# Kernel optimization log

Measured on AMD Instinct MI355X. Metric: run time of the kernel, lower is better.

The kernel has to match this reference:

```python
import jax, jax.numpy as jnp
import numpy as np

B, T, D = 2, 2048, 1024
H, KVH, HD = 16, 4, 64  # query heads, kv heads, head_dim
GROUPS = H // KVH


def apply_rope(x, cos, sin):
    # x: (B, nh, T, hd); cos/sin: (max_T, hd//2)
    t = x.shape[2]
    c = cos[:t][None, None]  # (1,1,T,hd//2)
    s = sin[:t][None, None]
    half = x.shape[-1] // 2
    x1, x2 = x[..., :half], x[..., half:]
    rotated = jnp.concatenate((-x2, x1), axis=-1)
    cf = jnp.concatenate((c, c), axis=-1)  # repeat(1,1,1,2)
    sf = jnp.concatenate((s, s), axis=-1)
    return x * cf + rotated * sf


def setup_inputs():
    key = jax.random.key(0)
    ks = jax.random.split(key, 5)
    x = jax.random.normal(ks[0], (B, T, D), dtype=jnp.float32)
    # RoPE tables: theta^(-i/half) frequencies
    half = HD // 2
    inv_freq = 1.0 / (10000.0 ** (jnp.arange(half, dtype=jnp.float32) / half))
    ang = jnp.arange(T, dtype=jnp.float32)[:, None] * inv_freq[None, :]  # (T, half)
    rope_cos = jnp.cos(ang)
    rope_sin = jnp.sin(ang)
    # Causal additive mask
    causal = jnp.tril(jnp.ones((T, T), dtype=bool))
    attention_mask = jnp.where(causal, 0.0, -1e9).astype(jnp.float32)[None, None]
    scale = 0.02
    Wq = jax.random.normal(ks[1], (D, D), dtype=jnp.float32) * scale
    Wk = jax.random.normal(ks[2], (D, KVH * HD), dtype=jnp.float32) * scale
    Wv = jax.random.normal(ks[3], (D, KVH * HD), dtype=jnp.float32) * scale
    Wo = jax.random.normal(ks[4], (D, D), dtype=jnp.float32) * scale
    return {"x": x, "rope_cos": rope_cos, "rope_sin": rope_sin,
            "attention_mask": attention_mask,
            "Wq": Wq, "Wk": Wk, "Wv": Wv, "Wo": Wo}


def reference(x, rope_cos, rope_sin, attention_mask, Wq, Wk, Wv, Wo):
    b, t, _ = x.shape
    q = (x @ Wq).reshape(b, t, H, HD).transpose(0, 2, 1, 3)      # (B,H,T,hd)
    k = (x @ Wk).reshape(b, t, KVH, HD).transpose(0, 2, 1, 3)    # (B,KVH,T,hd)
    v = (x @ Wv).reshape(b, t, KVH, HD).transpose(0, 2, 1, 3)
    q = apply_rope(q, rope_cos, rope_sin)
    k = apply_rope(k, rope_cos, rope_sin)
    if GROUPS > 1:
        k = jnp.repeat(k, GROUPS, axis=1)  # repeat_interleave over heads
        v = jnp.repeat(v, GROUPS, axis=1)
    scale = 1.0 / np.sqrt(HD)
    attn = jnp.einsum('bhqd,bhkd->bhqk', q, k) * scale
    attn = attn + attention_mask
    attn = jax.nn.softmax(attn.astype(jnp.float32), axis=-1).astype(q.dtype)
    out = jnp.einsum('bhqk,bhkd->bhqd', attn, v)
    out = out.transpose(0, 2, 1, 3).reshape(b, t, D)
    return out @ Wo
```

## Files before the change

kernel.cpp:

```cpp
#include <hip/hip_runtime.h>

typedef __attribute__((ext_vector_type(8))) short short8;
typedef __attribute__((ext_vector_type(4))) short short4v;
typedef __attribute__((ext_vector_type(4))) float f32x4;
typedef __attribute__((ext_vector_type(16))) float f32x16;
typedef __attribute__((ext_vector_type(2))) unsigned uint2v;
typedef __attribute__((ext_vector_type(4))) unsigned uint4v;

#define T_ 2048
#define H_ 16
#define KVH_ 4
#define QSCALE 0.18033688011112042f
#define DEFER 8.0f

__device__ inline unsigned short f2bf(float f) {
    unsigned u = __builtin_bit_cast(unsigned, f);
    u += 0x7fff + ((u >> 16) & 1);
    return (unsigned short)(u >> 16);
}
__device__ inline float bf2f(unsigned short v) {
    unsigned u = ((unsigned)v) << 16;
    return __builtin_bit_cast(float, u);
}
__device__ inline unsigned pk2(float lo, float hi) {
    unsigned r;
    asm("v_cvt_pk_bf16_f32 %0, %1, %2" : "=v"(r) : "v"(lo), "v"(hi));
    return r;
}

__device__ inline void gl_lds16(const unsigned short* g, unsigned short* lds) {
    __builtin_amdgcn_global_load_lds(
        (const __attribute__((address_space(1))) unsigned int*)g,
        (__attribute__((address_space(3))) unsigned int*)lds, 16, 0, 0);
}

__device__ void tr_tile(const float* __restrict__ W, unsigned short* __restrict__ out,
                        int K, int N, int rowoff, int bx, int by, int tid,
                        unsigned short (*ts)[66]) {
    #pragma unroll
    for (int s = 0; s < 16; ++s) {
        int idx = tid + s * 256;
        int kl = idx >> 6, nl = idx & 63;
        ts[kl][nl] = f2bf(W[(size_t)(by * 64 + kl) * N + bx * 64 + nl]);
    }
    __syncthreads();
    #pragma unroll
    for (int s = 0; s < 16; ++s) {
        int idx = tid + s * 256;
        int nl = idx >> 6, kl = idx & 63;
        out[(size_t)(rowoff + bx * 64 + nl) * K + by * 64 + kl] = ts[kl][nl];
    }
}

__global__ __launch_bounds__(256) void prep_fused(
        const float* __restrict__ x,
        const float* __restrict__ Wq, const float* __restrict__ Wk,
        const float* __restrict__ Wv, const float* __restrict__ Wo,
        unsigned short* __restrict__ xb, unsigned short* __restrict__ Wt,
        unsigned short* __restrict__ Wot) {
    __shared__ unsigned short ts[64][66];
    const int bid = blockIdx.x, tid = threadIdx.x;
    if (bid < 2048) {
        int i = bid * 256 + tid;
        float4 v0 = ((const float4*)x)[i * 2];
        float4 v1 = ((const float4*)x)[i * 2 + 1];
        short8 o;
        o[0] = f2bf(v0.x); o[1] = f2bf(v0.y); o[2] = f2bf(v0.z); o[3] = f2bf(v0.w);
        o[4] = f2bf(v1.x); o[5] = f2bf(v1.y); o[6] = f2bf(v1.z); o[7] = f2bf(v1.w);
        ((short8*)xb)[i] = o;
    } else if (bid < 2304) {
        int t = bid - 2048;
        tr_tile(Wq, Wt, 1024, 1024, 0, t & 15, t >> 4, tid, ts);
    } else if (bid < 2368) {
        int t = bid - 2304;
        tr_tile(Wk, Wt, 1024, 256, 1024, t & 3, t >> 2, tid, ts);
    } else if (bid < 2432) {
        int t = bid - 2368;
        tr_tile(Wv, Wt, 1024, 256, 1280, t & 3, t >> 2, tid, ts);
    } else {
        int t = bid - 2432;
        tr_tile(Wo, Wot, 1024, 1024, 0, t & 15, t >> 4, tid, ts);
    }
}

__global__ __launch_bounds__(256) void gemm_qkv(
        const unsigned short* __restrict__ A,
        const unsigned short* __restrict__ Bt,
        unsigned short* __restrict__ Cq, unsigned short* __restrict__ Ck,
        unsigned short* __restrict__ Cvt,
        const float* __restrict__ rc, const float* __restrict__ rs) {
    const int K = 1024;
    __shared__ __align__(16) unsigned short As[128 * 32];
    __shared__ __align__(16) unsigned short Bs[128 * 32];
    const int tid = threadIdx.x;
    const int w = tid >> 6, l = tid & 63, lk = l & 15, lg = l >> 4;
    const int wr = w >> 1, wc = w & 1;
    const int bx = blockIdx.x, by = blockIdx.y;

    const unsigned short* Arow = A + (size_t)by * 128 * K;
    const unsigned short* Brow = Bt + (size_t)bx * 128 * K;

    f32x4 acc[4][4];
    #pragma unroll
    for (int m = 0; m < 4; ++m)
        #pragma unroll
        for (int n = 0; n < 4; ++n) acc[m][n] = (f32x4){0, 0, 0, 0};

    for (int k0 = 0; k0 < K; k0 += 32) {
        #pragma unroll
        for (int p = 0; p < 2; ++p) {
            int cb = w * 64 + p * 256;
            int c = cb + l;
            int row = c >> 2, ko = (c & 3) * 8;
            gl_lds16(Arow + (size_t)row * K + k0 + ko, As + cb * 8);
            gl_lds16(Brow + (size_t)row * K + k0 + ko, Bs + cb * 8);
        }
        __syncthreads();
        short8 aF[4], bF[4];
        #pragma unroll
        for (int m = 0; m < 4; ++m)
            aF[m] = *(const short8*)&As[(wr * 64 + m * 16 + lk) * 32 + lg * 8];
        #pragma unroll
        for (int n = 0; n < 4; ++n)
            bF[n] = *(const short8*)&Bs[(wc * 64 + n * 16 + lk) * 32 + lg * 8];
        #pragma unroll
        for (int m = 0; m < 4; ++m)
            #pragma unroll
            for (int n = 0; n < 4; ++n)
                acc[m][n] = __builtin_amdgcn_mfma_f32_16x16x32_bf16(
                    aF[m], bF[n], acc[m][n], 0, 0, 0);
        __syncthreads();
    }

    const int rowbase = by * 128 + wr * 64;
    const int colgrp = bx * 2 + wc;
    if (colgrp < 16) {
        const int h = colgrp;
        #pragma unroll
        for (int m = 0; m < 4; ++m)
            #pragma unroll
            for (int r = 0; r < 4; ++r) {
                int trow = rowbase + m * 16 + lg * 4 + r;
                int b = trow >> 11, t = trow & (T_ - 1);
                size_t ob = (((size_t)(b * 16 + h)) * T_ + t) * 64;
                #pragma unroll
                for (int n = 0; n < 2; ++n) {
                    int d = n * 16 + lk;
                    float cc = rc[t * 32 + d], ss = rs[t * 32 + d];
                    float x1 = acc[m][n][r], x2 = acc[m][n + 2][r];
                    Cq[ob + d]      = f2bf((x1 * cc - x2 * ss) * QSCALE);
                    Cq[ob + d + 32] = f2bf((x2 * cc + x1 * ss) * QSCALE);
                }
            }
    } else if (colgrp < 20) {
        const int kvh = colgrp - 16;
        #pragma unroll
        for (int m = 0; m < 4; ++m)
            #pragma unroll
            for (int r = 0; r < 4; ++r) {
                int trow = rowbase + m * 16 + lg * 4 + r;
                int b = trow >> 11, t = trow & (T_ - 1);
                size_t ob = (((size_t)(b * 4 + kvh)) * T_ + t) * 64;
                #pragma unroll
                for (int n = 0; n < 2; ++n) {
                    int d = n * 16 + lk;
                    float cc = rc[t * 32 + d], ss = rs[t * 32 + d];
                    float x1 = acc[m][n][r], x2 = acc[m][n + 2][r];
                    Ck[ob + d]      = f2bf(x1 * cc - x2 * ss);
                    Ck[ob + d + 32] = f2bf(x2 * cc + x1 * ss);
                }
            }
    } else {
        const int kvh = colgrp - 20;
        #pragma unroll
        for (int m = 0; m < 4; ++m) {
            int trow0 = rowbase + m * 16 + lg * 4;
            int b = trow0 >> 11, t0 = trow0 & (T_ - 1);
            #pragma unroll
            for (int n = 0; n < 4; ++n) {
                int d = n * 16 + lk;
                short4v pk;
                #pragma unroll
                for (int r = 0; r < 4; ++r) pk[r] = f2bf(acc[m][n][r]);
                *(short4v*)(Cvt + (((size_t)(b * 4 + kvh)) * 64 + d) * T_ + t0) = pk;
            }
        }
    }
}

__global__ __launch_bounds__(256) void gemm_o(
        const unsigned short* __restrict__ A,
        const unsigned short* __restrict__ Bt,
        float* __restrict__ C, int M, int N, int K) {
    __shared__ __align__(16) unsigned short As[128 * 32];
    __shared__ __align__(16) unsigned short Bs[64 * 32];
    const int tid = threadIdx.x;
    const int w = tid >> 6, l = tid & 63, lk = l & 15, lg = l >> 4;
    const int bx = blockIdx.x, by = blockIdx.y;

    const unsigned short* Arow = A + (size_t)by * 128 * K;
    const unsigned short* Brow = Bt + (size_t)bx * 64 * K;

    f32x4 acc[2][4];
    #pragma unroll
    for (int m = 0; m < 2; ++m)
        #pragma unroll
        for (int n = 0; n < 4; ++n) acc[m][n] = (f32x4){0, 0, 0, 0};

    for (int k0 = 0; k0 < K; k0 += 32) {
        #pragma unroll
        for (int p = 0; p < 2; ++p) {
            int cb = p * 256 + w * 64;
            int c = cb + l;
            int row = c >> 2, ko = (c & 3) * 8;
            gl_lds16(Arow + (size_t)row * K + k0 + ko, As + cb * 8);
        }
        {
            int c = w * 64 + l;
            int row = c >> 2, ko = (c & 3) * 8;
            gl_lds16(Brow + (size_t)row * K + k0 + ko, Bs + c * 8);
        }
        __syncthreads();
        short8 aF[2], bF[4];
        #pragma unroll
        for (int m = 0; m < 2; ++m)
            aF[m] = *(const short8*)&As[(w * 32 + m * 16 + lk) * 32 + lg * 8];
        #pragma unroll
        for (int n = 0; n < 4; ++n)
            bF[n] = *(const short8*)&Bs[(n * 16 + lk) * 32 + lg * 8];
        #pragma unroll
        for (int m = 0; m < 2; ++m)
            #pragma unroll
            for (int n = 0; n < 4; ++n)
                acc[m][n] = __builtin_amdgcn_mfma_f32_16x16x32_bf16(
                    aF[m], bF[n], acc[m][n], 0, 0, 0);
        __syncthreads();
    }

    const int rowbase = by * 128 + w * 32;
    #pragma unroll
    for (int m = 0; m < 2; ++m)
        #pragma unroll
        for (int r = 0; r < 4; ++r) {
            size_t ro = (size_t)(rowbase + m * 16 + lg * 4 + r) * N + bx * 64 + lk;
            #pragma unroll
            for (int n = 0; n < 4; ++n) C[ro + n * 16] = acc[m][n][r];
        }
}

#define SWC(row, col) ((col) ^ (((row) & 7) << 3))
#define CROW(r, hi) (((r) & 3) + 8 * ((r) >> 2) + 4 * (hi))

__global__ __launch_bounds__(256) void attn_mfma(
        const unsigned short* __restrict__ Q,
        const unsigned short* __restrict__ K,
        const unsigned short* __restrict__ Vt,
        unsigned short* __restrict__ O,
        float* __restrict__ PM, float* __restrict__ PLp,
        unsigned short* __restrict__ PACC) {
    __shared__ __align__(16) unsigned short Ks[2][64 * 64];
    __shared__ __align__(16) unsigned short Vs[2][64 * 64];

    const int bid = blockIdx.x;
    int bh, qt, kt0, ktend, ck;
    bool direct;
    if (bid < 256) {
        bh = bid & 31; qt = 8 + (bid >> 5);
        kt0 = 0; ktend = 16; ck = 0; direct = false;
    } else if (bid < 512) {
        int j = bid - 256;
        bh = j & 31; qt = 7 - (j >> 5);
        kt0 = 0; ktend = 2 * qt + 2; ck = 0; direct = true;
    } else {
        int j = bid - 512;
        bh = j & 31; qt = 15 - (j >> 5);
        kt0 = 16; ktend = 2 * qt + 2; ck = 1; direct = false;
    }
    const int nkt = ktend - kt0;
    const int h = bh & 15, b = bh >> 4, kv = h >> 2;
    const int tid = threadIdx.x;
    const int w = tid >> 6, l = tid & 63;
    const int q32 = l & 31, hi = l >> 5;

    const unsigned short* Kb = K + ((size_t)(b * 4 + kv)) * T_ * 64;
    const unsigned short* Vb = Vt + ((size_t)(b * 4 + kv)) * 64 * T_;

    short8 qf[4];
    {
        const unsigned short* qp =
            Q + (((size_t)(b * 16 + h)) * T_ + qt * 128 + w * 32 + q32) * 64 + hi * 8;
        #pragma unroll
        for (int s = 0; s < 4; ++s) qf[s] = *(const short8*)(qp + 16 * s);
    }

    f32x16 o0, o1;
    #pragma unroll
    for (int i = 0; i < 16; ++i) { o0[i] = 0.f; o1[i] = 0.f; }
    float mloc = -1e38f, lsum = 0.f;

    const int sr = l >> 3, sg = l & 7;
    auto stage = [&](int buf, int kt) {
        #pragma unroll
        for (int p = 0; p < 2; ++p) {
            const int ch = w * 2 + p;
            const int row = ch * 8 + sr;
            const int gs = (sg ^ sr) * 8;
            gl_lds16(Kb + ((size_t)(kt * 64 + row)) * 64 + gs, &Ks[buf][ch * 512]);
            gl_lds16(Vb + (size_t)row * T_ + kt * 64 + gs,     &Vs[buf][ch * 512]);
        }
    };

    auto mk = [&](float e0, float e1, float e2, float e3,
                  float e4, float e5, float e6, float e7) -> short8 {
        unsigned a0 = pk2(e0, e1);
        unsigned b0 = pk2(e4, e5);
        uint2v r02 = __builtin_amdgcn_permlane32_swap(a0, b0, false, false);
        unsigned a1 = pk2(e2, e3);
        unsigned b1 = pk2(e6, e7);
        uint2v r13 = __builtin_amdgcn_permlane32_swap(a1, b1, false, false);
        uint4v u;
        u[0] = r02[0]; u[1] = r13[0]; u[2] = r02[1]; u[3] = r13[1];
        return __builtin_bit_cast(short8, u);
    };

    stage(0, kt0);
    for (int i = 0; i < nkt; ++i) {
        const int kt = kt0 + i;
        const int cur = i & 1;
        __syncthreads();
        if (i + 1 < nkt) stage(cur ^ 1, kt0 + i + 1);

        f32x16 st0, st1;
        #pragma unroll
        for (int r = 0; r < 16; ++r) { st0[r] = 0.f; st1[r] = 0.f; }
        __builtin_amdgcn_s_setprio(1);
        #pragma unroll
        for (int s = 0; s < 4; ++s) {
            const int c = 16 * s + hi * 8;
            const int kr0 = q32, kr1 = 32 + q32;
            short8 k0 = *(const short8*)&Ks[cur][kr0 * 64 + SWC(kr0, c)];
            short8 k1 = *(const short8*)&Ks[cur][kr1 * 64 + SWC(kr1, c)];
            st0 = __builtin_amdgcn_mfma_f32_32x32x16_bf16(k0, qf[s], st0, 0, 0, 0);
            st1 = __builtin_amdgcn_mfma_f32_32x32x16_bf16(k1, qf[s], st1, 0, 0, 0);
        }
        __builtin_amdgcn_s_setprio(0);

        if (kt >= 2 * qt) {
            const int qg = qt * 128 + w * 32 + q32;
            #pragma unroll
            for (int r = 0; r < 16; ++r) {
                const int kg = kt * 64 + CROW(r, hi);
                if (kg > qg)      st0[r] = -1e30f;
                if (kg + 32 > qg) st1[r] = -1e30f;
            }
        }

        float tm[16];
        #pragma unroll
        for (int r = 0; r < 16; ++r) tm[r] = fmaxf(st0[r], st1[r]);
        #pragma unroll
        for (int d = 8; d >= 1; d >>= 1)
            #pragma unroll
            for (int r = 0; r < d; ++r) tm[r] = fmaxf(tm[r], tm[r + d]);
        float pm = fmaxf(tm[0], __shfl_xor(tm[0], 32));

        if (__any(pm > mloc + DEFER)) {
            const float nm = fmaxf(mloc, pm);
            const float corr = exp2f(mloc - nm);
            mloc = nm;
            lsum *= corr;
            #pragma unroll
            for (int r = 0; r < 16; ++r) {
                const float cr = __shfl(corr, CROW(r, hi));
                o0[r] *= cr;
                o1[r] *= cr;
            }
        }

        float ts[16];
        #pragma unroll
        for (int r = 0; r < 16; ++r) {
            st0[r] = exp2f(st0[r] - mloc);
            st1[r] = exp2f(st1[r] - mloc);
            ts[r] = st0[r] + st1[r];
        }
        #pragma unroll
        for (int d = 8; d >= 1; d >>= 1)
            #pragma unroll
            for (int r = 0; r < d; ++r) ts[r] += ts[r + d];
        lsum += ts[0] + __shfl_xor(ts[0], 32);

        short8 pa0 = mk(st0[0], st0[1], st0[2],  st0[3],  st0[4],  st0[5],  st0[6],  st0[7]);
        short8 pa1 = mk(st0[8], st0[9], st0[10], st0[11], st0[12], st0[13], st0[14], st0[15]);
        short8 pa2 = mk(st1[0], st1[1], st1[2],  st1[3],  st1[4],  st1[5],  st1[6],  st1[7]);
        short8 pa3 = mk(st1[8], st1[9], st1[10], st1[11], st1[12], st1[13], st1[14], st1[15]);

        __builtin_amdgcn_s_setprio(1);
        const int vd0 = q32, vd1 = 32 + q32;
        #pragma unroll
        for (int ks = 0; ks < 4; ++ks) {
            short8 paf = (ks == 0) ? pa0 : (ks == 1) ? pa1 : (ks == 2) ? pa2 : pa3;
            const int c = 16 * ks + hi * 8;
            short8 vb0 = *(const short8*)&Vs[cur][vd0 * 64 + SWC(vd0, c)];
            short8 vb1 = *(const short8*)&Vs[cur][vd1 * 64 + SWC(vd1, c)];
            o0 = __builtin_amdgcn_mfma_f32_32x32x16_bf16(paf, vb0, o0, 0, 0, 0);
            o1 = __builtin_amdgcn_mfma_f32_32x32x16_bf16(paf, vb1, o1, 0, 0, 0);
        }
        __builtin_amdgcn_s_setprio(0);
    }

    if (direct) {
        #pragma unroll
        for (int r = 0; r < 16; ++r) {
            const float inv = 1.f / __shfl(lsum, CROW(r, hi));
            const int t = qt * 128 + w * 32 + CROW(r, hi);
            unsigned short* op = &O[(((size_t)(b * T_ + t)) * 16 + h) * 64 + q32];
            op[0]  = f2bf(o0[r] * inv);
            op[32] = f2bf(o1[r] * inv);
        }
    } else {
        const int p = ((bh << 3) + (qt - 8)) * 2 + ck;
        if (l < 32) {
            PM[p * 128 + w * 32 + l]  = mloc;
            PLp[p * 128 + w * 32 + l] = lsum;
        }
        #pragma unroll
        for (int r = 0; r < 16; ++r) {
            const int row = w * 32 + CROW(r, hi);
            unsigned short* pp = &PACC[((size_t)p * 128 + row) * 64 + q32];
            pp[0]  = f2bf(o0[r]);
            pp[32] = f2bf(o1[r]);
        }
    }
}

__global__ __launch_bounds__(256) void combine_attn(
        const float* __restrict__ PM, const float* __restrict__ PLp,
        const unsigned short* __restrict__ PACC,
        unsigned short* __restrict__ O) {
    const int cid = blockIdx.x;
    const int bh = cid & 31, qt = 8 + (cid >> 5);
    const int h = bh & 15, b = bh >> 4;
    const int tid = threadIdx.x;
    const int row = tid >> 1, cg = (tid & 1) * 32;
    const int p0 = ((bh << 3) + (qt - 8)) * 2, p1 = p0 + 1;

    float mA = PM[p0 * 128 + row], mB = PM[p1 * 128 + row];
    float lA = PLp[p0 * 128 + row], lB = PLp[p1 * 128 + row];
    float M = fmaxf(mA, mB);
    float wA = exp2f(mA - M), wB = exp2f(mB - M);
    float inv = 1.f / (lA * wA + lB * wB);
    wA *= inv; wB *= inv;

    const unsigned short* a = &PACC[((size_t)p0 * 128 + row) * 64 + cg];
    const unsigned short* c = &PACC[((size_t)p1 * 128 + row) * 64 + cg];
    int t = qt * 128 + row;
    unsigned short* op = &O[(((size_t)(b * T_ + t)) * 16 + h) * 64 + cg];
    #pragma unroll
    for (int j = 0; j < 4; ++j) {
        short8 va = *(const short8*)(a + j * 8);
        short8 vb = *(const short8*)(c + j * 8);
        short8 o;
        #pragma unroll
        for (int i = 0; i < 8; ++i)
            o[i] = f2bf(bf2f((unsigned short)va[i]) * wA +
                        bf2f((unsigned short)vb[i]) * wB);
        *(short8*)(op + j * 8) = o;
    }
}

extern "C" void kernel_launch(void* const* d_in, const int* in_sizes, int n_in,
                              void* d_out, int out_size, void* d_ws, size_t ws_size,
                              hipStream_t stream) {
    const float* x  = (const float*)d_in[0];
    const float* rc = (const float*)d_in[1];
    const float* rs = (const float*)d_in[2];
    const float* Wq = (const float*)d_in[4];
    const float* Wk = (const float*)d_in[5];
    const float* Wv = (const float*)d_in[6];
    const float* Wo = (const float*)d_in[7];
    float* out = (float*)d_out;

    unsigned short* ws = (unsigned short*)d_ws;
    unsigned short* xb  = ws;
    unsigned short* Wt  = ws + 4194304;
    unsigned short* Wot = ws + 5767168;
    unsigned short* Qbf = ws + 6815744;
    unsigned short* Kbf = ws + 11010048;
    unsigned short* Vtb = ws + 12058624;
    unsigned short* Ob  = ws + 13107200;

    float* PM            = (float*)d_ws;
    float* PLp           = PM + 512 * 128;
    unsigned short* PACC = (unsigned short*)(PLp + 512 * 128);

    dim3 blk(256);
    prep_fused<<<dim3(2688), blk, 0, stream>>>(x, Wq, Wk, Wv, Wo, xb, Wt, Wot);

    gemm_qkv<<<dim3(12, 32), blk, 0, stream>>>(xb, Wt, Qbf, Kbf, Vtb, rc, rs);

    attn_mfma<<<dim3(768), blk, 0, stream>>>(Qbf, Kbf, Vtb, Ob, PM, PLp, PACC);
    combine_attn<<<dim3(256), blk, 0, stream>>>(PM, PLp, PACC, Ob);

    gemm_o<<<dim3(16, 32), blk, 0, stream>>>(Ob, Wot, out, 4096, 1024, 1024);
}
```

Measured before the change: 114.5 us.

## Load K/V MFMA fragments directly from global memory, dropping LDS staging

The attention kernel no longer stages K and V tiles into double-buffered shared memory with async global-to-LDS copies and barriers. Each wave now loads its MFMA operand fragments for K and V straight from global memory every iteration. This removes the LDS traffic and __syncthreads, but the four waves in a block each fetch the same tiles redundantly through cache. The loads are also no longer prefetched a tile ahead, so global latency is exposed inside the loop.

```diff
diff --git a/kernel.cpp b/kernel.cpp
--- a/kernel.cpp
+++ b/kernel.cpp
@@ -248,7 +248,6 @@
         }
 }
 
-#define SWC(row, col) ((col) ^ (((row) & 7) << 3))
 #define CROW(r, hi) (((r) & 3) + 8 * ((r) >> 2) + 4 * (hi))
 
 __global__ __launch_bounds__(256) void attn_mfma(
@@ -258,9 +257,6 @@
         unsigned short* __restrict__ O,
         float* __restrict__ PM, float* __restrict__ PLp,
         unsigned short* __restrict__ PACC) {
-    __shared__ __align__(16) unsigned short Ks[2][64 * 64];
-    __shared__ __align__(16) unsigned short Vs[2][64 * 64];
-
     const int bid = blockIdx.x;
     int bh, qt, kt0, ktend, ck;
     bool direct;
@@ -284,6 +280,10 @@
 
     const unsigned short* Kb = K + ((size_t)(b * 4 + kv)) * T_ * 64;
     const unsigned short* Vb = Vt + ((size_t)(b * 4 + kv)) * 64 * T_;
+    const unsigned short* Kf0 = Kb + (size_t)q32 * 64 + hi * 8;
+    const unsigned short* Kf1 = Kb + (size_t)(32 + q32) * 64 + hi * 8;
+    const unsigned short* Vf0 = Vb + (size_t)q32 * T_ + hi * 8;
+    const unsigned short* Vf1 = Vb + (size_t)(32 + q32) * T_ + hi * 8;
 
     short8 qf[4];
     {
@@ -297,18 +297,6 @@
     #pragma unroll
     for (int i = 0; i < 16; ++i) { o0[i] = 0.f; o1[i] = 0.f; }
     float mloc = -1e38f, lsum = 0.f;
-
-    const int sr = l >> 3, sg = l & 7;
-    auto stage = [&](int buf, int kt) {
-        #pragma unroll
-        for (int p = 0; p < 2; ++p) {
-            const int ch = w * 2 + p;
-            const int row = ch * 8 + sr;
-            const int gs = (sg ^ sr) * 8;
-            gl_lds16(Kb + ((size_t)(kt * 64 + row)) * 64 + gs, &Ks[buf][ch * 512]);
-            gl_lds16(Vb + (size_t)row * T_ + kt * 64 + gs,     &Vs[buf][ch * 512]);
-        }
-    };
 
     auto mk = [&](float e0, float e1, float e2, float e3,
                   float e4, float e5, float e6, float e7) -> short8 {
@@ -323,12 +311,15 @@
         return __builtin_bit_cast(short8, u);
     };
 
-    stage(0, kt0);
     for (int i = 0; i < nkt; ++i) {
         const int kt = kt0 + i;
-        const int cur = i & 1;
-        __syncthreads();
-        if (i + 1 < nkt) stage(cur ^ 1, kt0 + i + 1);
+
+        short8 kf0[4], kf1[4];
+        #pragma unroll
+        for (int s = 0; s < 4; ++s) {
+            kf0[s] = *(const short8*)(Kf0 + (size_t)kt * 4096 + 16 * s);
+            kf1[s] = *(const short8*)(Kf1 + (size_t)kt * 4096 + 16 * s);
+        }
 
         f32x16 st0, st1;
         #pragma unroll
@@ -336,14 +327,17 @@
         __builtin_amdgcn_s_setprio(1);
         #pragma unroll
         for (int s = 0; s < 4; ++s) {
-            const int c = 16 * s + hi * 8;
-            const int kr0 = q32, kr1 = 32 + q32;
-            short8 k0 = *(const short8*)&Ks[cur][kr0 * 64 + SWC(kr0, c)];
-            short8 k1 = *(const short8*)&Ks[cur][kr1 * 64 + SWC(kr1, c)];
-            st0 = __builtin_amdgcn_mfma_f32_32x32x16_bf16(k0, qf[s], st0, 0, 0, 0);
-            st1 = __builtin_amdgcn_mfma_f32_32x32x16_bf16(k1, qf[s], st1, 0, 0, 0);
+            st0 = __builtin_amdgcn_mfma_f32_32x32x16_bf16(kf0[s], qf[s], st0, 0, 0, 0);
+            st1 = __builtin_amdgcn_mfma_f32_32x32x16_bf16(kf1[s], qf[s], st1, 0, 0, 0);
         }
         __builtin_amdgcn_s_setprio(0);
+
+        short8 vf0[4], vf1[4];
+        #pragma unroll
+        for (int ks = 0; ks < 4; ++ks) {
+            vf0[ks] = *(const short8*)(Vf0 + kt * 64 + 16 * ks);
+            vf1[ks] = *(const short8*)(Vf1 + kt * 64 + 16 * ks);
+        }
 
         if (kt >= 2 * qt) {
             const int qg = qt * 128 + w * 32 + q32;
@@ -396,15 +390,11 @@
         short8 pa3 = mk(st1[8], st1[9], st1[10], st1[11], st1[12], st1[13], st1[14], st1[15]);
 
         __builtin_amdgcn_s_setprio(1);
-        const int vd0 = q32, vd1 = 32 + q32;
         #pragma unroll
         for (int ks = 0; ks < 4; ++ks) {
             short8 paf = (ks == 0) ? pa0 : (ks == 1) ? pa1 : (ks == 2) ? pa2 : pa3;
-            const int c = 16 * ks + hi * 8;
-            short8 vb0 = *(const short8*)&Vs[cur][vd0 * 64 + SWC(vd0, c)];
-            short8 vb1 = *(const short8*)&Vs[cur][vd1 * 64 + SWC(vd1, c)];
-            o0 = __builtin_amdgcn_mfma_f32_32x32x16_bf16(paf, vb0, o0, 0, 0, 0);
-            o1 = __builtin_amdgcn_mfma_f32_32x32x16_bf16(paf, vb1, o1, 0, 0, 0);
+            o0 = __builtin_amdgcn_mfma_f32_32x32x16_bf16(paf, vf0[ks], o0, 0, 0, 0);
+            o1 = __builtin_amdgcn_mfma_f32_32x32x16_bf16(paf, vf1[ks], o1, 0, 0, 0);
         }
         __builtin_amdgcn_s_setprio(0);
     }
```

New measurement: 139.0 us. 1.21x slower.
